# Performance work log

Measured on AMD Instinct MI355X. Metric: run time of the kernel, lower is better.

## Reference

```python
import jax, jax.numpy as jnp
import numpy as np

B, S, D, N = 8, 4096, 1024, 16
EPS = 1e-6


def setup_inputs() -> dict:
    key = jax.random.key(0)
    ks = jax.random.split(key, 6)
    s = 1.0 / np.sqrt(D)
    return {
        "x": jax.random.normal(ks[0], (B, S, D), dtype=jnp.float32),
        "W_lambda": jax.random.uniform(ks[1], (N, D), jnp.float32, -s, s),
        "b_lambda": jnp.full((N,), 2.0, dtype=jnp.float32),  # nn.init.constant_(bias, 2.0)
        "W_B": jax.random.uniform(ks[2], (N, D), jnp.float32, -s, s),
        "W_C": jax.random.uniform(ks[3], (D, N), jnp.float32, -1.0 / np.sqrt(N), 1.0 / np.sqrt(N)),
        "W_gate": jax.random.uniform(ks[4], (D, D), jnp.float32, -s, s),
        "rms_weight": jnp.ones((D,), dtype=jnp.float32),
    }


def reference(x, W_lambda, b_lambda, W_B, W_C, W_gate, rms_weight):
    # Input-dependent decay and input projection, computed for all timesteps at once
    lam = jax.nn.sigmoid(jnp.einsum("bsd,nd->bsn", x, W_lambda) + b_lambda)  # (B,S,N)
    Bx = jnp.einsum("bsd,nd->bsn", x, W_B)  # (B,S,N)

    def step(h, inp):
        l_t, b_t = inp
        h = l_t * h + b_t  # h_t = lambda_t * h_{t-1} + B_t x_t
        return h, h

    h0 = jnp.zeros((x.shape[0], W_B.shape[0]), dtype=x.dtype)
    _, hs = jax.lax.scan(step, h0, (jnp.swapaxes(lam, 0, 1), jnp.swapaxes(Bx, 0, 1)))
    hs = jnp.swapaxes(hs, 0, 1)  # (B,S,N)

    y = jnp.einsum("bsn,dn->bsd", hs, W_C)  # C @ h_t
    gate = jax.nn.sigmoid(jnp.einsum("bsd,ed->bse", x, W_gate))
    y = gate * y
    # RMSNorm
    rms = jax.lax.rsqrt(jnp.mean(y * y, axis=-1, keepdims=True) + EPS)
    return y * rms * rms_weight
```

## Files before the change

### kernel.cpp

```cpp
#include <hip/hip_runtime.h>

#define DD 1024
#define NN 16
#define SS 4096
#define BBATCH 8
#define TOK (BBATCH*SS)

typedef __attribute__((ext_vector_type(8))) __bf16 bf16x8;
typedef __attribute__((ext_vector_type(4))) __bf16 bf16x4;
typedef __attribute__((ext_vector_type(4))) float f32x4;
typedef unsigned int u32;
typedef unsigned long long u64;

__device__ __forceinline__ void async16(void* lds, const void* g) {
  __builtin_amdgcn_global_load_lds(
      (const __attribute__((address_space(1))) u32*)(u64)(g),
      (__attribute__((address_space(3))) u32*)(u32)(u64)(lds), 16, 0, 0);
}

__device__ __forceinline__ float sigmoidf_(float v) {
  return 1.f / (1.f + __expf(-v));
}

__global__ void k_cvtw(const float* __restrict__ wgf, const float* __restrict__ wlf,
                       const float* __restrict__ wbf, __bf16* __restrict__ wg,
                       __bf16* __restrict__ wp) {
  int i = blockIdx.x * blockDim.x + threadIdx.x;
  const int NG = DD * DD / 8, NP = NN * DD / 8;
  const float* src; __bf16* dst;
  if (i < NG)           { src = wgf + (u64)i * 8;            dst = wg + (u64)i * 8; }
  else if (i < NG + NP) { int j = i - NG; src = wlf + j * 8; dst = wp + j * 8; }
  else if (i < NG + 2 * NP) { int j = i - NG - NP; src = wbf + j * 8; dst = wp + NN * DD + j * 8; }
  else return;
  float4 a = *(const float4*)src, b = *(const float4*)(src + 4);
  bf16x8 o;
  o[0] = (__bf16)a.x; o[1] = (__bf16)a.y; o[2] = (__bf16)a.z; o[3] = (__bf16)a.w;
  o[4] = (__bf16)b.x; o[5] = (__bf16)b.y; o[6] = (__bf16)b.z; o[7] = (__bf16)b.w;
  *(bf16x8*)dst = o;
}

__global__ __launch_bounds__(256)
void k_proj(const float* __restrict__ x, const __bf16* __restrict__ wp,
            const float* __restrict__ b_lambda, __bf16* __restrict__ xb,
            float* __restrict__ lam, float* __restrict__ bx) {
  __shared__ __align__(16) __bf16 sA[128 * 32];
  __shared__ __align__(16) __bf16 sB[32 * 32];
  int tid = threadIdx.x;
  int lane = tid & 63, w = tid >> 6;
  int tok0 = blockIdx.x * 128;
  int crow = tid >> 1, cs = (tid & 1) * 2;
  const float* xsrc = x + (u64)(tok0 + crow) * DD + (tid & 1) * 16;
  __bf16* xdst = xb + (u64)(tok0 + crow) * DD + (tid & 1) * 16;
  int sw = (crow & 3) ^ ((crow >> 2) & 3);
  u64 bSrc;
  {
    int u = tid;
    int row = u >> 2, slot = (u & 3) ^ (row & 3);
    bSrc = (u64)((const char*)wp + ((u64)row * DD + slot * 8) * 2);
  }
  f32x4 acc[2][2] = {};
  int r15 = lane & 15, kg = lane >> 4;
  for (int kt = 0; kt < DD / 32; ++kt) {
    float4 a0 = *(const float4*)(xsrc + kt * 32 + 0);
    float4 a1 = *(const float4*)(xsrc + kt * 32 + 4);
    float4 a2 = *(const float4*)(xsrc + kt * 32 + 8);
    float4 a3 = *(const float4*)(xsrc + kt * 32 + 12);
    bf16x8 lo, hi;
    lo[0] = (__bf16)a0.x; lo[1] = (__bf16)a0.y; lo[2] = (__bf16)a0.z; lo[3] = (__bf16)a0.w;
    lo[4] = (__bf16)a1.x; lo[5] = (__bf16)a1.y; lo[6] = (__bf16)a1.z; lo[7] = (__bf16)a1.w;
    hi[0] = (__bf16)a2.x; hi[1] = (__bf16)a2.y; hi[2] = (__bf16)a2.z; hi[3] = (__bf16)a2.w;
    hi[4] = (__bf16)a3.x; hi[5] = (__bf16)a3.y; hi[6] = (__bf16)a3.z; hi[7] = (__bf16)a3.w;
    *(bf16x8*)(xdst + kt * 32) = lo;
    *(bf16x8*)(xdst + kt * 32 + 8) = hi;
    *(bf16x8*)((char*)sA + crow * 64 + ((cs ^ sw) << 4)) = lo;
    *(bf16x8*)((char*)sA + crow * 64 + (((cs + 1) ^ sw) << 4)) = hi;
    if (tid < 128)
      async16((char*)sB + w * 1024, (const void*)(bSrc + kt * 64));
    __syncthreads();
    bf16x8 bfr[2];
#pragma unroll
    for (int nt = 0; nt < 2; ++nt) {
      int brow = nt * 16 + r15;
      bfr[nt] = *(const bf16x8*)((const char*)sB + brow * 64 + ((kg ^ (brow & 3)) << 4));
    }
#pragma unroll
    for (int mt = 0; mt < 2; ++mt) {
      int arow = w * 32 + mt * 16 + r15;
      bf16x8 af = *(const bf16x8*)((const char*)sA + arow * 64 +
                                   ((kg ^ (arow & 3) ^ ((arow >> 2) & 3)) << 4));
#pragma unroll
      for (int nt = 0; nt < 2; ++nt)
        acc[mt][nt] = __builtin_amdgcn_mfma_f32_16x16x32_bf16(af, bfr[nt], acc[mt][nt], 0, 0, 0);
    }
    __syncthreads();
  }
#pragma unroll
  for (int mt = 0; mt < 2; ++mt)
#pragma unroll
    for (int nt = 0; nt < 2; ++nt)
#pragma unroll
      for (int r = 0; r < 4; ++r) {
        int token = tok0 + w * 32 + mt * 16 + kg * 4 + r;
        int j = nt * 16 + r15;
        float v = acc[mt][nt][r];
        if (j < 16) lam[token * NN + j] = sigmoidf_(v + b_lambda[j]);
        else        bx[token * NN + (j - 16)] = v;
      }
}

__global__ __launch_bounds__(256)
void k_scan(const float* __restrict__ lam, const float* __restrict__ bx,
            float* __restrict__ hs) {
  int b = blockIdx.x >> 4, n = blockIdx.x & 15;
  int t = threadIdx.x;
  const int CH = SS / 256;
  float lv[CH], bv[CH];
  int base = (b * SS + t * CH) * NN + n;
  float a = 1.f, bacc = 0.f;
#pragma unroll
  for (int i = 0; i < CH; ++i) {
    lv[i] = lam[base + i * NN];
    bv[i] = bx[base + i * NN];
    bacc = lv[i] * bacc + bv[i];
    a *= lv[i];
  }
  __shared__ float As[2][256], Bs[2][256];
  As[0][t] = a; Bs[0][t] = bacc;
  __syncthreads();
  int cur = 0;
  for (int off = 1; off < 256; off <<= 1) {
    float a2 = As[cur][t], b2 = Bs[cur][t];
    if (t >= off) {
      float ap = As[cur][t - off], bp = Bs[cur][t - off];
      b2 = b2 + a2 * bp;
      a2 = a2 * ap;
    }
    As[cur ^ 1][t] = a2; Bs[cur ^ 1][t] = b2;
    cur ^= 1;
    __syncthreads();
  }
  float h = (t == 0) ? 0.f : Bs[cur][t - 1];
#pragma unroll
  for (int i = 0; i < CH; ++i) {
    h = lv[i] * h + bv[i];
    hs[base + i * NN] = h;
  }
}

#define STAGE(tile, M, h) do {                                                    \
    u32 lds0 = (u32)(((((tile) & 1) * 4 + (M) * 2 + (h)) << 14) + tid * 16);      \
    u64 g0 = ((M) ? bBase : aBase) + ((u64)(h) << 18) + (u64)(tile) * 128;        \
    async16(smc + lds0, (const void*)g0);                                         \
    async16(smc + lds0 + 8192, (const void*)(g0 + 131072));                       \
  } while (0)

template<int YB16>
__global__ __launch_bounds__(512, 2)
void k_gemm(const __bf16* __restrict__ xb, const __bf16* __restrict__ wg,
            const float* __restrict__ hs, const float* __restrict__ wc,
            float* __restrict__ outf, __bf16* __restrict__ outb) {
  __shared__ __align__(16) char smc[131072];
  const int tid = threadIdx.x, lane = tid & 63, w = tid >> 6;
  const int r15 = lane & 15, kg = lane >> 4;
  const int wr = w >> 2, wcq = w & 3;
  int bid = blockIdx.x;
  int swz = (bid & 7) * 64 + (bid >> 3);
  int m = swz >> 2, n = swz & 3;
  const int tok0 = m * 256, n0 = n * 256;
  const int sslot = (tid & 7) ^ ((tid >> 3) & 7);
  const u64 aBase = (u64)(const char*)xb + (u64)(tok0 + (tid >> 3)) * 2048 + (u32)sslot * 16;
  const u64 bBase = (u64)(const char*)wg + (u64)(n0 + (tid >> 3)) * 2048 + (u32)sslot * 16;
  const u32 sxa0 = (u32)(((0 | kg) ^ (r15 & 7)) * 16);
  const u32 sxa1 = (u32)(((4 | kg) ^ (r15 & 7)) * 16);
  const u32 lrB0 = (u32)((wcq & 1) * 64);

  f32x4 acc[8][4] = {};

  STAGE(0, 0, 0); STAGE(0, 0, 1); STAGE(0, 1, 0); STAGE(0, 1, 1);
  STAGE(1, 1, 0); STAGE(1, 1, 1); STAGE(1, 0, 0);
  asm volatile("s_waitcnt vmcnt(6)" ::: "memory");
  __builtin_amdgcn_s_barrier();
  asm volatile("" ::: "memory");

  for (int k = 0; k < 16; ++k) {
    const int b = k & 1;
    const char* Ah = smc + (u32)((b * 4 + wr) << 14);
    const char* Bh = smc + (u32)((b * 4 + 2 + (wcq >> 1)) << 14);
    bf16x8 af[8][2], bfr[4][2];
#pragma unroll
    for (int mt = 0; mt < 2; ++mt) {
      u32 ro = (u32)(mt * 16 + r15) * 128;
      af[mt][0] = *(const bf16x8*)(Ah + ro + sxa0);
      af[mt][1] = *(const bf16x8*)(Ah + ro + sxa1);
    }
#pragma unroll
    for (int nt = 0; nt < 4; ++nt) {
      u32 ro = (lrB0 + (u32)(nt * 16 + r15)) * 128;
      bfr[nt][0] = *(const bf16x8*)(Bh + ro + sxa0);
      bfr[nt][1] = *(const bf16x8*)(Bh + ro + sxa1);
    }
    if (k <= 14) STAGE(k + 1, 0, 1);
    __builtin_amdgcn_s_barrier();
    asm volatile("s_waitcnt lgkmcnt(0)" ::: "memory");
    __builtin_amdgcn_sched_barrier(0);
    __builtin_amdgcn_s_setprio(1);
#pragma unroll
    for (int mt = 0; mt < 2; ++mt)
#pragma unroll
      for (int nt = 0; nt < 4; ++nt) {
        acc[mt][nt] = __builtin_amdgcn_mfma_f32_16x16x32_bf16(af[mt][0], bfr[nt][0], acc[mt][nt], 0, 0, 0);
        acc[mt][nt] = __builtin_amdgcn_mfma_f32_16x16x32_bf16(af[mt][1], bfr[nt][1], acc[mt][nt], 0, 0, 0);
      }
    __builtin_amdgcn_s_setprio(0);
    __builtin_amdgcn_s_barrier();
    asm volatile("" ::: "memory");
#pragma unroll
    for (int mt = 2; mt < 6; ++mt) {
      u32 ro = (u32)(mt * 16 + r15) * 128;
      af[mt][0] = *(const bf16x8*)(Ah + ro + sxa0);
      af[mt][1] = *(const bf16x8*)(Ah + ro + sxa1);
    }
    if (k <= 13) STAGE(k + 2, 1, 0);
    __builtin_amdgcn_s_barrier();
    asm volatile("s_waitcnt lgkmcnt(0)" ::: "memory");
    __builtin_amdgcn_sched_barrier(0);
    __builtin_amdgcn_s_setprio(1);
#pragma unroll
    for (int mt = 2; mt < 4; ++mt)
#pragma unroll
      for (int nt = 0; nt < 4; ++nt) {
        acc[mt][nt] = __builtin_amdgcn_mfma_f32_16x16x32_bf16(af[mt][0], bfr[nt][0], acc[mt][nt], 0, 0, 0);
        acc[mt][nt] = __builtin_amdgcn_mfma_f32_16x16x32_bf16(af[mt][1], bfr[nt][1], acc[mt][nt], 0, 0, 0);
      }
    __builtin_amdgcn_s_setprio(0);
    __builtin_amdgcn_s_barrier();
    asm volatile("" ::: "memory");
#pragma unroll
    for (int mt = 6; mt < 8; ++mt) {
      u32 ro = (u32)(mt * 16 + r15) * 128;
      af[mt][0] = *(const bf16x8*)(Ah + ro + sxa0);
      af[mt][1] = *(const bf16x8*)(Ah + ro + sxa1);
    }
    if (k <= 13) STAGE(k + 2, 1, 1);
    __builtin_amdgcn_s_barrier();
    asm volatile("s_waitcnt lgkmcnt(0)" ::: "memory");
    __builtin_amdgcn_sched_barrier(0);
    __builtin_amdgcn_s_setprio(1);
#pragma unroll
    for (int mt = 4; mt < 6; ++mt)
#pragma unroll
      for (int nt = 0; nt < 4; ++nt) {
        acc[mt][nt] = __builtin_amdgcn_mfma_f32_16x16x32_bf16(af[mt][0], bfr[nt][0], acc[mt][nt], 0, 0, 0);
        acc[mt][nt] = __builtin_amdgcn_mfma_f32_16x16x32_bf16(af[mt][1], bfr[nt][1], acc[mt][nt], 0, 0, 0);
      }
    __builtin_amdgcn_s_setprio(0);
    __builtin_amdgcn_s_barrier();
    asm volatile("" ::: "memory");
    if (k <= 13) STAGE(k + 2, 0, 0);
    if (k <= 13)      asm volatile("s_waitcnt vmcnt(6)" ::: "memory");
    else if (k == 14) asm volatile("s_waitcnt vmcnt(0)" ::: "memory");
    __builtin_amdgcn_s_barrier();
    asm volatile("" ::: "memory");
    __builtin_amdgcn_s_setprio(1);
#pragma unroll
    for (int mt = 6; mt < 8; ++mt)
#pragma unroll
      for (int nt = 0; nt < 4; ++nt) {
        acc[mt][nt] = __builtin_amdgcn_mfma_f32_16x16x32_bf16(af[mt][0], bfr[nt][0], acc[mt][nt], 0, 0, 0);
        acc[mt][nt] = __builtin_amdgcn_mfma_f32_16x16x32_bf16(af[mt][1], bfr[nt][1], acc[mt][nt], 0, 0, 0);
      }
    __builtin_amdgcn_s_setprio(0);
  }
  asm volatile("" ::: "memory");

  __bf16* hsH = (__bf16*)smc;
  __bf16* hsL = (__bf16*)(smc + 16384);
  __bf16* wcB = (__bf16*)(smc + 32768);
  {
    int row = tid >> 1, half = tid & 1;
    const float* hp = hs + (u64)(tok0 + row) * NN + half * 8;
    const float* wp2 = wc + (u64)(n0 + row) * NN + half * 8;
    float4 h0 = *(const float4*)hp, h1 = *(const float4*)(hp + 4);
    float4 w0 = *(const float4*)wp2, w1 = *(const float4*)(wp2 + 4);
    bf16x8 hh, hl, wb, zz = {};
    float hv[8] = {h0.x, h0.y, h0.z, h0.w, h1.x, h1.y, h1.z, h1.w};
    float wv[8] = {w0.x, w0.y, w0.z, w0.w, w1.x, w1.y, w1.z, w1.w};
#pragma unroll
    for (int e = 0; e < 8; ++e) {
      __bf16 hi = (__bf16)hv[e];
      hh[e] = hi;
      hl[e] = (__bf16)(hv[e] - (float)hi);
      wb[e] = (__bf16)wv[e];
    }
    u32 realOff = (u32)row * 32 + (u32)((half ^ (row & 3)) << 3);
    u32 zeroOff = (u32)row * 32 + (u32)(((2 + half) ^ (row & 3)) << 3);
    *(bf16x8*)(hsH + realOff) = hh;  *(bf16x8*)(hsH + zeroOff) = zz;
    *(bf16x8*)(hsL + realOff) = hl;  *(bf16x8*)(hsL + zeroOff) = zz;
    *(bf16x8*)(wcB + realOff) = wb;  *(bf16x8*)(wcB + zeroOff) = zz;
  }
  __syncthreads();
  bf16x8 bw[4];
#pragma unroll
  for (int nt = 0; nt < 4; ++nt) {
    int row = wcq * 64 + nt * 16 + r15;
    bw[nt] = *(const bf16x8*)(wcB + row * 32 + ((kg ^ (row & 3)) << 3));
  }
  const f32x4 zero4 = {};
#pragma unroll
  for (int mt = 0; mt < 8; ++mt) {
    int arow = wr * 128 + mt * 16 + r15;
    u32 ao = (u32)arow * 32 + (u32)((kg ^ (arow & 3)) << 3);
    bf16x8 ah = *(const bf16x8*)(hsH + ao);
    bf16x8 al = *(const bf16x8*)(hsL + ao);
#pragma unroll
    for (int nt = 0; nt < 4; ++nt) {
      f32x4 cy4 = __builtin_amdgcn_mfma_f32_16x16x32_bf16(al, bw[nt], zero4, 0, 0, 0);
      cy4 = __builtin_amdgcn_mfma_f32_16x16x32_bf16(ah, bw[nt], cy4, 0, 0, 0);
      int j = wcq * 64 + nt * 16 + r15;
#pragma unroll
      for (int r = 0; r < 4; ++r) {
        int i = wr * 128 + mt * 16 + kg * 4 + r;
        float g = sigmoidf_(acc[mt][nt][r]);
        u64 off = (u64)(tok0 + i) * DD + n0 + j;
        if (YB16) outb[off] = (__bf16)(g * cy4[r]);
        else      outf[off] = g * cy4[r];
      }
    }
  }
}

__global__ __launch_bounds__(256)
void k_norm_b(const __bf16* __restrict__ yb, float* __restrict__ out,
              const float* __restrict__ rw) {
  int row = blockIdx.x * 4 + (threadIdx.x >> 6);
  int lane = threadIdx.x & 63;
  const __bf16* yrow = yb + (u64)row * DD;
  bf16x4 v[4];
  float f[16];
  float rs = 0.f;
#pragma unroll
  for (int q = 0; q < 4; ++q) {
    v[q] = *(const bf16x4*)(yrow + q * 256 + lane * 4);
#pragma unroll
    for (int e = 0; e < 4; ++e) {
      f[q * 4 + e] = (float)v[q][e];
      rs += f[q * 4 + e] * f[q * 4 + e];
    }
  }
#pragma unroll
  for (int msk = 1; msk < 64; msk <<= 1) rs += __shfl_xor(rs, msk, 64);
  float rstd = rsqrtf(rs * (1.f / DD) + 1e-6f);
  float* orow = out + (u64)row * DD;
#pragma unroll
  for (int q = 0; q < 4; ++q) {
    float4 wv = *(const float4*)(rw + q * 256 + lane * 4);
    float4 o;
    o.x = f[q * 4 + 0] * rstd * wv.x;
    o.y = f[q * 4 + 1] * rstd * wv.y;
    o.z = f[q * 4 + 2] * rstd * wv.z;
    o.w = f[q * 4 + 3] * rstd * wv.w;
    *(float4*)(orow + q * 256 + lane * 4) = o;
  }
}

__global__ __launch_bounds__(256)
void k_norm_f(float* __restrict__ out, const float* __restrict__ rw) {
  int row = blockIdx.x * 4 + (threadIdx.x >> 6);
  int lane = threadIdx.x & 63;
  float4* p = (float4*)(out + (u64)row * DD);
  float4 v[4];
  float rs = 0.f;
#pragma unroll
  for (int e = 0; e < 4; ++e) {
    v[e] = p[e * 64 + lane];
    rs += v[e].x * v[e].x + v[e].y * v[e].y + v[e].z * v[e].z + v[e].w * v[e].w;
  }
#pragma unroll
  for (int msk = 1; msk < 64; msk <<= 1) rs += __shfl_xor(rs, msk, 64);
  float rstd = rsqrtf(rs * (1.f / DD) + 1e-6f);
  const float4* rwp = (const float4*)rw;
#pragma unroll
  for (int e = 0; e < 4; ++e) {
    float4 wv = rwp[e * 64 + lane];
    float4 o;
    o.x = v[e].x * rstd * wv.x;
    o.y = v[e].y * rstd * wv.y;
    o.z = v[e].z * rstd * wv.z;
    o.w = v[e].w * rstd * wv.w;
    p[e * 64 + lane] = o;
  }
}

extern "C" void kernel_launch(void* const* d_in, const int* in_sizes, int n_in,
                              void* d_out, int out_size, void* d_ws, size_t ws_size,
                              hipStream_t stream) {
  (void)in_sizes; (void)n_in; (void)out_size;
  const float* x        = (const float*)d_in[0];
  const float* W_lambda = (const float*)d_in[1];
  const float* b_lambda = (const float*)d_in[2];
  const float* W_B      = (const float*)d_in[3];
  const float* W_C      = (const float*)d_in[4];
  const float* W_gate   = (const float*)d_in[5];
  const float* rms_w    = (const float*)d_in[6];
  char* ws = (char*)d_ws;
  __bf16* xb  = (__bf16*)(ws + 0);
  __bf16* wg  = (__bf16*)(ws + 67108864);
  __bf16* wp  = (__bf16*)(ws + 69206016);
  float*  lam = (float*)(ws + 69271552);
  float*  bx  = (float*)(ws + 71368704);
  float*  hs  = (float*)(ws + 73465856);
  __bf16* yb  = (__bf16*)(ws + 75563008);
  float*  out = (float*)d_out;
  bool yb16 = ws_size >= (size_t)(75563008ull + 67108864ull);

  k_cvtw<<<(DD * DD / 8 + 2 * NN * DD / 8 + 255) / 256, 256, 0, stream>>>(
      W_gate, W_lambda, W_B, wg, wp);
  k_proj<<<TOK / 128, 256, 0, stream>>>(x, wp, b_lambda, xb, lam, bx);
  k_scan<<<BBATCH * NN, 256, 0, stream>>>(lam, bx, hs);
  if (yb16) {
    k_gemm<1><<<(TOK / 256) * (DD / 256), 512, 0, stream>>>(xb, wg, hs, W_C, nullptr, yb);
    k_norm_b<<<TOK / 4, 256, 0, stream>>>(yb, out, rms_w);
  } else {
    k_gemm<0><<<(TOK / 256) * (DD / 256), 512, 0, stream>>>(xb, wg, hs, W_C, out, nullptr);
    k_norm_f<<<TOK / 4, 256, 0, stream>>>(out, rms_w);
  }
}
```

Measured before the change: 188.8 us.

## Fold W_gate conversion into scan launch and coarsen GEMM main-loop pipeline

The W_gate fp32-to-bf16 conversion moves out of the pre-projection conversion kernel and into extra blocks of the scan kernel, which otherwise launches only 128 blocks and leaves most CUs idle. The GEMM main loop is restructured from four sub-phases with staggered staging to two halves: each half loads four A sub-tiles and issues two stages, which cuts barriers per iteration and changes the prefetch depth. The cost is less overlap between LDS reads, global loads and MFMAs, a changed wait-count pattern, and higher register pressure from holding more fragments at once.

```diff
diff --git a/kernel.cpp b/kernel.cpp
--- a/kernel.cpp
+++ b/kernel.cpp
@@ -22,15 +22,13 @@
   return 1.f / (1.f + __expf(-v));
 }
 
-__global__ void k_cvtw(const float* __restrict__ wgf, const float* __restrict__ wlf,
-                       const float* __restrict__ wbf, __bf16* __restrict__ wg,
+__global__ void k_cvtw(const float* __restrict__ wlf, const float* __restrict__ wbf,
                        __bf16* __restrict__ wp) {
   int i = blockIdx.x * blockDim.x + threadIdx.x;
-  const int NG = DD * DD / 8, NP = NN * DD / 8;
+  const int NP = NN * DD / 8;
   const float* src; __bf16* dst;
-  if (i < NG)           { src = wgf + (u64)i * 8;            dst = wg + (u64)i * 8; }
-  else if (i < NG + NP) { int j = i - NG; src = wlf + j * 8; dst = wp + j * 8; }
-  else if (i < NG + 2 * NP) { int j = i - NG - NP; src = wbf + j * 8; dst = wp + NN * DD + j * 8; }
+  if (i < NP)            { src = wlf + (u64)i * 8;            dst = wp + (u64)i * 8; }
+  else if (i < 2 * NP)   { int j = i - NP; src = wbf + (u64)j * 8; dst = wp + NN * DD + (u64)j * 8; }
   else return;
   float4 a = *(const float4*)src, b = *(const float4*)(src + 4);
   bf16x8 o;
@@ -110,7 +108,18 @@
 
 __global__ __launch_bounds__(256)
 void k_scan(const float* __restrict__ lam, const float* __restrict__ bx,
-            float* __restrict__ hs) {
+            float* __restrict__ hs, const float* __restrict__ wgf,
+            __bf16* __restrict__ wg) {
+  if (blockIdx.x >= BBATCH * NN) {
+    int i = (blockIdx.x - BBATCH * NN) * 256 + threadIdx.x;
+    const float* src = wgf + (u64)i * 8;
+    float4 a = *(const float4*)src, b = *(const float4*)(src + 4);
+    bf16x8 o;
+    o[0] = (__bf16)a.x; o[1] = (__bf16)a.y; o[2] = (__bf16)a.z; o[3] = (__bf16)a.w;
+    o[4] = (__bf16)b.x; o[5] = (__bf16)b.y; o[6] = (__bf16)b.z; o[7] = (__bf16)b.w;
+    *(bf16x8*)(wg + (u64)i * 8) = o;
+    return;
+  }
   int b = blockIdx.x >> 4, n = blockIdx.x & 15;
   int t = threadIdx.x;
   const int CH = SS / 256;
@@ -177,8 +186,8 @@
   f32x4 acc[8][4] = {};
 
   STAGE(0, 0, 0); STAGE(0, 0, 1); STAGE(0, 1, 0); STAGE(0, 1, 1);
-  STAGE(1, 1, 0); STAGE(1, 1, 1); STAGE(1, 0, 0);
-  asm volatile("s_waitcnt vmcnt(6)" ::: "memory");
+  STAGE(1, 1, 0); STAGE(1, 1, 1);
+  asm volatile("s_waitcnt vmcnt(4)" ::: "memory");
   __builtin_amdgcn_s_barrier();
   asm volatile("" ::: "memory");
 
@@ -188,7 +197,7 @@
     const char* Bh = smc + (u32)((b * 4 + 2 + (wcq >> 1)) << 14);
     bf16x8 af[8][2], bfr[4][2];
 #pragma unroll
-    for (int mt = 0; mt < 2; ++mt) {
+    for (int mt = 0; mt < 4; ++mt) {
       u32 ro = (u32)(mt * 16 + r15) * 128;
       af[mt][0] = *(const bf16x8*)(Ah + ro + sxa0);
       af[mt][1] = *(const bf16x8*)(Ah + ro + sxa1);
@@ -199,13 +208,13 @@
       bfr[nt][0] = *(const bf16x8*)(Bh + ro + sxa0);
       bfr[nt][1] = *(const bf16x8*)(Bh + ro + sxa1);
     }
-    if (k <= 14) STAGE(k + 1, 0, 1);
+    if (k <= 14) { STAGE(k + 1, 0, 0); STAGE(k + 1, 0, 1); }
     __builtin_amdgcn_s_barrier();
     asm volatile("s_waitcnt lgkmcnt(0)" ::: "memory");
     __builtin_amdgcn_sched_barrier(0);
     __builtin_amdgcn_s_setprio(1);
 #pragma unroll
-    for (int mt = 0; mt < 2; ++mt)
+    for (int mt = 0; mt < 4; ++mt)
 #pragma unroll
       for (int nt = 0; nt < 4; ++nt) {
         acc[mt][nt] = __builtin_amdgcn_mfma_f32_16x16x32_bf16(af[mt][0], bfr[nt][0], acc[mt][nt], 0, 0, 0);
@@ -215,63 +224,29 @@
     __builtin_amdgcn_s_barrier();
     asm volatile("" ::: "memory");
 #pragma unroll
-    for (int mt = 2; mt < 6; ++mt) {
+    for (int mt = 4; mt < 8; ++mt) {
       u32 ro = (u32)(mt * 16 + r15) * 128;
       af[mt][0] = *(const bf16x8*)(Ah + ro + sxa0);
       af[mt][1] = *(const bf16x8*)(Ah + ro + sxa1);
     }
-    if (k <= 13) STAGE(k + 2, 1, 0);
+    if (k <= 13) { STAGE(k + 2, 1, 0); STAGE(k + 2, 1, 1); }
     __builtin_amdgcn_s_barrier();
     asm volatile("s_waitcnt lgkmcnt(0)" ::: "memory");
     __builtin_amdgcn_sched_barrier(0);
     __builtin_amdgcn_s_setprio(1);
 #pragma unroll
-    for (int mt = 2; mt < 4; ++mt)
+    for (int mt = 4; mt < 8; ++mt)
 #pragma unroll
       for (int nt = 0; nt < 4; ++nt) {
         acc[mt][nt] = __builtin_amdgcn_mfma_f32_16x16x32_bf16(af[mt][0], bfr[nt][0], acc[mt][nt], 0, 0, 0);
         acc[mt][nt] = __builtin_amdgcn_mfma_f32_16x16x32_bf16(af[mt][1], bfr[nt][1], acc[mt][nt], 0, 0, 0);
       }
     __builtin_amdgcn_s_setprio(0);
-    __builtin_amdgcn_s_barrier();
-    asm volatile("" ::: "memory");
-#pragma unroll
-    for (int mt = 6; mt < 8; ++mt) {
-      u32 ro = (u32)(mt * 16 + r15) * 128;
-      af[mt][0] = *(const bf16x8*)(Ah + ro + sxa0);
-      af[mt][1] = *(const bf16x8*)(Ah + ro + sxa1);
-    }
-    if (k <= 13) STAGE(k + 2, 1, 1);
-    __builtin_amdgcn_s_barrier();
-    asm volatile("s_waitcnt lgkmcnt(0)" ::: "memory");
-    __builtin_amdgcn_sched_barrier(0);
-    __builtin_amdgcn_s_setprio(1);
-#pragma unroll
-    for (int mt = 4; mt < 6; ++mt)
-#pragma unroll
-      for (int nt = 0; nt < 4; ++nt) {
-        acc[mt][nt] = __builtin_amdgcn_mfma_f32_16x16x32_bf16(af[mt][0], bfr[nt][0], acc[mt][nt], 0, 0, 0);
-        acc[mt][nt] = __builtin_amdgcn_mfma_f32_16x16x32_bf16(af[mt][1], bfr[nt][1], acc[mt][nt], 0, 0, 0);
-      }
-    __builtin_amdgcn_s_setprio(0);
-    __builtin_amdgcn_s_barrier();
-    asm volatile("" ::: "memory");
-    if (k <= 13) STAGE(k + 2, 0, 0);
-    if (k <= 13)      asm volatile("s_waitcnt vmcnt(6)" ::: "memory");
+    if (k <= 13)      asm volatile("s_waitcnt vmcnt(4)" ::: "memory");
     else if (k == 14) asm volatile("s_waitcnt vmcnt(0)" ::: "memory");
     __builtin_amdgcn_s_barrier();
     asm volatile("" ::: "memory");
-    __builtin_amdgcn_s_setprio(1);
-#pragma unroll
-    for (int mt = 6; mt < 8; ++mt)
-#pragma unroll
-      for (int nt = 0; nt < 4; ++nt) {
-        acc[mt][nt] = __builtin_amdgcn_mfma_f32_16x16x32_bf16(af[mt][0], bfr[nt][0], acc[mt][nt], 0, 0, 0);
-        acc[mt][nt] = __builtin_amdgcn_mfma_f32_16x16x32_bf16(af[mt][1], bfr[nt][1], acc[mt][nt], 0, 0, 0);
-      }
-    __builtin_amdgcn_s_setprio(0);
-  }
-  asm volatile("" ::: "memory");
+  }
 
   __bf16* hsH = (__bf16*)smc;
   __bf16* hsL = (__bf16*)(smc + 16384);
@@ -413,10 +388,9 @@
   float*  out = (float*)d_out;
   bool yb16 = ws_size >= (size_t)(75563008ull + 67108864ull);
 
-  k_cvtw<<<(DD * DD / 8 + 2 * NN * DD / 8 + 255) / 256, 256, 0, stream>>>(
-      W_gate, W_lambda, W_B, wg, wp);
+  k_cvtw<<<(2 * NN * DD / 8 + 255) / 256, 256, 0, stream>>>(W_lambda, W_B, wp);
   k_proj<<<TOK / 128, 256, 0, stream>>>(x, wp, b_lambda, xb, lam, bx);
-  k_scan<<<BBATCH * NN, 256, 0, stream>>>(lam, bx, hs);
+  k_scan<<<BBATCH * NN + DD * DD / 8 / 256, 256, 0, stream>>>(lam, bx, hs, W_gate, wg);
   if (yb16) {
     k_gemm<1><<<(TOK / 256) * (DD / 256), 512, 0, stream>>>(xb, wg, hs, W_C, nullptr, yb);
     k_norm_b<<<TOK / 4, 256, 0, stream>>>(yb, out, rms_w);
```

New measurement: 189.8 us. Within noise of the previous version (+0.5%).

## Shrink projection tiles to 32 tokens and fold W_gate conversion into scan launch

Applied to the files above, without the earlier changes.

The projection kernel now handles 32 tokens per block instead of 128, launching four times as many blocks. Each wave computes a single 16x16 MFMA tile and each thread converts one float4 of x per k-step. This is meant to raise occupancy and memory parallelism in the bandwidth-bound pass over x. Separately, the W_gate fp32-to-bf16 conversion moves out of the small up-front kernel into extra blocks of the scan launch, so it overlaps with the latency-bound scan instead of delaying the projection. The cost is more blocks, more barriers per token and narrower global loads.

```diff
diff --git a/kernel.cpp b/kernel.cpp
--- a/kernel.cpp
+++ b/kernel.cpp
@@ -22,15 +22,13 @@
   return 1.f / (1.f + __expf(-v));
 }
 
-__global__ void k_cvtw(const float* __restrict__ wgf, const float* __restrict__ wlf,
-                       const float* __restrict__ wbf, __bf16* __restrict__ wg,
+__global__ void k_cvtw(const float* __restrict__ wlf, const float* __restrict__ wbf,
                        __bf16* __restrict__ wp) {
   int i = blockIdx.x * blockDim.x + threadIdx.x;
-  const int NG = DD * DD / 8, NP = NN * DD / 8;
+  const int NP = NN * DD / 8;
   const float* src; __bf16* dst;
-  if (i < NG)           { src = wgf + (u64)i * 8;            dst = wg + (u64)i * 8; }
-  else if (i < NG + NP) { int j = i - NG; src = wlf + j * 8; dst = wp + j * 8; }
-  else if (i < NG + 2 * NP) { int j = i - NG - NP; src = wbf + j * 8; dst = wp + NN * DD + j * 8; }
+  if (i < NP)            { src = wlf + (u64)i * 8;            dst = wp + (u64)i * 8; }
+  else if (i < 2 * NP)   { int j = i - NP; src = wbf + (u64)j * 8; dst = wp + NN * DD + (u64)j * 8; }
   else return;
   float4 a = *(const float4*)src, b = *(const float4*)(src + 4);
   bf16x8 o;
@@ -43,74 +41,66 @@
 void k_proj(const float* __restrict__ x, const __bf16* __restrict__ wp,
             const float* __restrict__ b_lambda, __bf16* __restrict__ xb,
             float* __restrict__ lam, float* __restrict__ bx) {
-  __shared__ __align__(16) __bf16 sA[128 * 32];
+  __shared__ __align__(16) __bf16 sA[32 * 32];
   __shared__ __align__(16) __bf16 sB[32 * 32];
   int tid = threadIdx.x;
   int lane = tid & 63, w = tid >> 6;
-  int tok0 = blockIdx.x * 128;
-  int crow = tid >> 1, cs = (tid & 1) * 2;
-  const float* xsrc = x + (u64)(tok0 + crow) * DD + (tid & 1) * 16;
-  __bf16* xdst = xb + (u64)(tok0 + crow) * DD + (tid & 1) * 16;
-  int sw = (crow & 3) ^ ((crow >> 2) & 3);
-  u64 bSrc;
-  {
-    int u = tid;
-    int row = u >> 2, slot = (u & 3) ^ (row & 3);
+  int tok0 = blockIdx.x * 32;
+  int r15 = lane & 15, kg = lane >> 4;
+  int mt = w >> 1;
+  int crow = tid >> 3, coff = (tid & 7) * 4;
+  const float* xsrc = x + (u64)(tok0 + crow) * DD + coff;
+  __bf16* xdst = xb + (u64)(tok0 + crow) * DD + coff;
+  u32 aoff = (u32)crow * 64 +
+             ((u32)((coff >> 3) ^ (crow & 3) ^ ((crow >> 2) & 3)) << 4) +
+             ((coff & 4) ? 8u : 0u);
+  u64 bSrc = 0;
+  if (tid < 128) {
+    int u = tid, row = u >> 2, slot = (u & 3) ^ (row & 3);
     bSrc = (u64)((const char*)wp + ((u64)row * DD + slot * 8) * 2);
   }
-  f32x4 acc[2][2] = {};
-  int r15 = lane & 15, kg = lane >> 4;
+  f32x4 acc = {};
+  int arow = mt * 16 + r15;
+  u32 aro = (u32)arow * 64 + ((u32)(kg ^ (arow & 3) ^ ((arow >> 2) & 3)) << 4);
+  int brow = (w & 1) * 16 + r15;
+  u32 bro = (u32)brow * 64 + ((u32)(kg ^ (brow & 3)) << 4);
   for (int kt = 0; kt < DD / 32; ++kt) {
-    float4 a0 = *(const float4*)(xsrc + kt * 32 + 0);
-    float4 a1 = *(const float4*)(xsrc + kt * 32 + 4);
-    float4 a2 = *(const float4*)(xsrc + kt * 32 + 8);
-    float4 a3 = *(const float4*)(xsrc + kt * 32 + 12);
-    bf16x8 lo, hi;
-    lo[0] = (__bf16)a0.x; lo[1] = (__bf16)a0.y; lo[2] = (__bf16)a0.z; lo[3] = (__bf16)a0.w;
-    lo[4] = (__bf16)a1.x; lo[5] = (__bf16)a1.y; lo[6] = (__bf16)a1.z; lo[7] = (__bf16)a1.w;
-    hi[0] = (__bf16)a2.x; hi[1] = (__bf16)a2.y; hi[2] = (__bf16)a2.z; hi[3] = (__bf16)a2.w;
-    hi[4] = (__bf16)a3.x; hi[5] = (__bf16)a3.y; hi[6] = (__bf16)a3.z; hi[7] = (__bf16)a3.w;
-    *(bf16x8*)(xdst + kt * 32) = lo;
-    *(bf16x8*)(xdst + kt * 32 + 8) = hi;
-    *(bf16x8*)((char*)sA + crow * 64 + ((cs ^ sw) << 4)) = lo;
-    *(bf16x8*)((char*)sA + crow * 64 + (((cs + 1) ^ sw) << 4)) = hi;
+    float4 a0 = *(const float4*)(xsrc + kt * 32);
+    bf16x4 cv;
+    cv[0] = (__bf16)a0.x; cv[1] = (__bf16)a0.y; cv[2] = (__bf16)a0.z; cv[3] = (__bf16)a0.w;
+    *(bf16x4*)(xdst + kt * 32) = cv;
+    *(bf16x4*)((char*)sA + aoff) = cv;
     if (tid < 128)
-      async16((char*)sB + w * 1024, (const void*)(bSrc + kt * 64));
+      async16((char*)sB + (tid >> 6) * 1024, (const void*)(bSrc + kt * 64));
     __syncthreads();
-    bf16x8 bfr[2];
-#pragma unroll
-    for (int nt = 0; nt < 2; ++nt) {
-      int brow = nt * 16 + r15;
-      bfr[nt] = *(const bf16x8*)((const char*)sB + brow * 64 + ((kg ^ (brow & 3)) << 4));
-    }
-#pragma unroll
-    for (int mt = 0; mt < 2; ++mt) {
-      int arow = w * 32 + mt * 16 + r15;
-      bf16x8 af = *(const bf16x8*)((const char*)sA + arow * 64 +
-                                   ((kg ^ (arow & 3) ^ ((arow >> 2) & 3)) << 4));
-#pragma unroll
-      for (int nt = 0; nt < 2; ++nt)
-        acc[mt][nt] = __builtin_amdgcn_mfma_f32_16x16x32_bf16(af, bfr[nt], acc[mt][nt], 0, 0, 0);
-    }
+    bf16x8 af = *(const bf16x8*)((const char*)sA + aro);
+    bf16x8 bfr = *(const bf16x8*)((const char*)sB + bro);
+    acc = __builtin_amdgcn_mfma_f32_16x16x32_bf16(af, bfr, acc, 0, 0, 0);
     __syncthreads();
   }
-#pragma unroll
-  for (int mt = 0; mt < 2; ++mt)
-#pragma unroll
-    for (int nt = 0; nt < 2; ++nt)
-#pragma unroll
-      for (int r = 0; r < 4; ++r) {
-        int token = tok0 + w * 32 + mt * 16 + kg * 4 + r;
-        int j = nt * 16 + r15;
-        float v = acc[mt][nt][r];
-        if (j < 16) lam[token * NN + j] = sigmoidf_(v + b_lambda[j]);
-        else        bx[token * NN + (j - 16)] = v;
-      }
+  float bl = b_lambda[r15];
+#pragma unroll
+  for (int r = 0; r < 4; ++r) {
+    int token = tok0 + mt * 16 + kg * 4 + r;
+    if ((w & 1) == 0) lam[token * NN + r15] = sigmoidf_(acc[r] + bl);
+    else              bx[token * NN + r15] = acc[r];
+  }
 }
 
 __global__ __launch_bounds__(256)
 void k_scan(const float* __restrict__ lam, const float* __restrict__ bx,
-            float* __restrict__ hs) {
+            float* __restrict__ hs, const float* __restrict__ wgf,
+            __bf16* __restrict__ wg) {
+  if (blockIdx.x >= BBATCH * NN) {
+    int i = (blockIdx.x - BBATCH * NN) * 256 + threadIdx.x;
+    const float* src = wgf + (u64)i * 8;
+    float4 a = *(const float4*)src, b = *(const float4*)(src + 4);
+    bf16x8 o;
+    o[0] = (__bf16)a.x; o[1] = (__bf16)a.y; o[2] = (__bf16)a.z; o[3] = (__bf16)a.w;
+    o[4] = (__bf16)b.x; o[5] = (__bf16)b.y; o[6] = (__bf16)b.z; o[7] = (__bf16)b.w;
+    *(bf16x8*)(wg + (u64)i * 8) = o;
+    return;
+  }
   int b = blockIdx.x >> 4, n = blockIdx.x & 15;
   int t = threadIdx.x;
   const int CH = SS / 256;
@@ -413,10 +403,9 @@
   float*  out = (float*)d_out;
   bool yb16 = ws_size >= (size_t)(75563008ull + 67108864ull);
 
-  k_cvtw<<<(DD * DD / 8 + 2 * NN * DD / 8 + 255) / 256, 256, 0, stream>>>(
-      W_gate, W_lambda, W_B, wg, wp);
-  k_proj<<<TOK / 128, 256, 0, stream>>>(x, wp, b_lambda, xb, lam, bx);
-  k_scan<<<BBATCH * NN, 256, 0, stream>>>(lam, bx, hs);
+  k_cvtw<<<(2 * NN * DD / 8 + 255) / 256, 256, 0, stream>>>(W_lambda, W_B, wp);
+  k_proj<<<TOK / 32, 256, 0, stream>>>(x, wp, b_lambda, xb, lam, bx);
+  k_scan<<<BBATCH * NN + DD * DD / 8 / 256, 256, 0, stream>>>(lam, bx, hs, W_gate, wg);
   if (yb16) {
     k_gemm<1><<<(TOK / 256) * (DD / 256), 512, 0, stream>>>(xb, wg, hs, W_C, nullptr, yb);
     k_norm_b<<<TOK / 4, 256, 0, stream>>>(yb, out, rms_w);
```

Measured after the change: 189.2 us. Within noise of the previous version (+0.2%).
